# Kernel optimization log

Hardware: AMD Instinct MI355X
Metric: run time of the kernel (lower is better)

Reference implementation:

```python
import jax, jax.numpy as jnp
import numpy as np

# sign with straight-through estimator: grad passes only where |input| < 1
@jax.custom_vjp
def sign_ste(x):
    return jnp.sign(x)

def _sign_ste_fwd(x):
    return jnp.sign(x), x

def _sign_ste_bwd(x, g):
    return (jnp.where(jnp.abs(x) < 1.0, g, jnp.zeros_like(g)),)

sign_ste.defvjp(_sign_ste_fwd, _sign_ste_bwd)

# weight binarization: torch mutates weight.data in-place, so autograd treats
# sign() as identity w.r.t. the weight variable (plain linear gradient)
@jax.custom_vjp
def sign_id(w):
    return jnp.sign(w)

def _sign_id_fwd(w):
    return jnp.sign(w), None

def _sign_id_bwd(_, g):
    return (g,)

sign_id.defvjp(_sign_id_fwd, _sign_id_bwd)


def setup_inputs() -> dict:
    key = jax.random.key(0)
    k1, k2, k3 = jax.random.split(key, 3)
    x = jax.random.normal(k1, (8192, 4096), dtype=jnp.float32)
    # weight initialized to random ±1 (bernoulli(0.5)*2-1), as in __init__
    W = jnp.sign(jax.random.normal(k2, (4096, 4096), dtype=jnp.float32))
    b = jax.random.normal(k3, (4096,), dtype=jnp.float32) * 0.02
    return {"x": x, "W": W, "b": b}


def reference(x, W, b):
    # x: [N, in]; W: [out, in]; b: [out]
    x_mean = jnp.mean(jnp.abs(x))          # scalar scale, differentiable
    xb = sign_ste(x)                        # ±1 activations, STE gradient
    wb = sign_id(W)                         # ±1 weights, identity gradient
    out = jnp.einsum('ni,oi->no', xb, wb) + b  # [N, out]
    return out * x_mean
```

## Files before the change

### kernel.cpp

```cpp
#include <hip/hip_runtime.h>

typedef int intx4 __attribute__((ext_vector_type(4)));
typedef int intx8 __attribute__((ext_vector_type(8)));
typedef float floatx4 __attribute__((ext_vector_type(4)));

#define M_DIM 8192
#define N_DIM 4096
#define K_DIM 4096
#define KB2 (K_DIM / 2)

#define PACK_BLOCKS 2048
#define NF4_X ((size_t)M_DIM * K_DIM / 4)
#define NF4_TOT (NF4_X + (size_t)N_DIM * K_DIM / 4)

__device__ __forceinline__ void gld_lds16(const char* g, char* l) {
  __builtin_amdgcn_global_load_lds(
      (const __attribute__((address_space(1))) unsigned int*)g,
      (__attribute__((address_space(3))) unsigned int*)l,
      16, 0, 0);
}

__device__ __forceinline__ unsigned nib(float v) {
  return v > 0.0f ? 0x2u : (v < 0.0f ? 0xAu : 0x0u);
}

__global__ __launch_bounds__(256) void pack_kernel(const float* __restrict__ x,
                                                   const float* __restrict__ Wm,
                                                   unsigned short* __restrict__ pk,
                                                   double* __restrict__ accd) {
  const int t = threadIdx.x;
  const size_t stride = (size_t)PACK_BLOCKS * 256;
  const float4* __restrict__ X4 = (const float4*)x;
  const float4* __restrict__ W4 = (const float4*)Wm;
  float s = 0.0f;
  for (size_t i = (size_t)blockIdx.x * 256 + t; i < NF4_TOT; i += stride) {
    float4 v;
    if (i < NF4_X) {
      v = X4[i];
      s += fabsf(v.x) + fabsf(v.y) + fabsf(v.z) + fabsf(v.w);
    } else {
      v = W4[i - NF4_X];
    }
    pk[i] = (unsigned short)(nib(v.x) | (nib(v.y) << 4) | (nib(v.z) << 8) |
                             (nib(v.w) << 12));
  }
  #pragma unroll
  for (int off = 32; off > 0; off >>= 1) s += __shfl_down(s, off);
  __shared__ float sp[4];
  if ((t & 63) == 0) sp[t >> 6] = s;
  __syncthreads();
  if (t == 0) atomicAdd(accd, (double)(sp[0] + sp[1] + sp[2] + sp[3]));
}

__global__ __launch_bounds__(256) void gemm_kernel(const char* __restrict__ Xb,
                                                   const char* __restrict__ Wb,
                                                   const float* __restrict__ bias,
                                                   const double* __restrict__ accd,
                                                   float* __restrict__ out) {
  __shared__ __align__(16) char lA[2][8192];
  __shared__ __align__(16) char lB[2][8192];
  const int t = threadIdx.x;
  const int lane = t & 63;
  const int w = t >> 6;
  const int m16 = lane & 15;
  const int quad = lane >> 4;
  const int bM = blockIdx.y * 128;
  const int bN = blockIdx.x * 128;
  const int waveM = (w & 1) * 64;
  const int waveN = (w >> 1) * 64;

  const int srl = 2 * (t >> 3) + (t & 1);
  const int ssc = (t >> 1) & 3;
  const int g0 = (ssc + (srl >> 1)) & 3;
  const char* gA = Xb + (size_t)(bM + srl) * KB2 + g0 * 16;
  const char* gB = Wb + (size_t)(bN + srl) * KB2 + g0 * 16;
  const int ldst = w * 1024;

  int offA[4], offB[4];
  #pragma unroll
  for (int i = 0; i < 4; ++i) {
    const int m = waveM + i * 16 + m16;
    offA[i] = (m >> 1) * 128 + (((quad - (m >> 1)) & 3)) * 32 + (m & 1) * 16;
    const int n = waveN + i * 16 + m16;
    offB[i] = (n >> 1) * 128 + (((quad - (n >> 1)) & 3)) * 32 + (n & 1) * 16;
  }

  floatx4 acc[4][4];
  #pragma unroll
  for (int i = 0; i < 4; ++i)
    #pragma unroll
    for (int j = 0; j < 4; ++j)
      acc[i][j] = (floatx4){0.0f, 0.0f, 0.0f, 0.0f};

#define STAGE(BUF, KB)                                                      \
  do {                                                                      \
    gld_lds16(gA + (KB), &lA[BUF][ldst]);                                   \
    gld_lds16(gA + (KB) + (size_t)64 * KB2, &lA[BUF][4096 + ldst]);         \
    gld_lds16(gB + (KB), &lB[BUF][ldst]);                                   \
    gld_lds16(gB + (KB) + (size_t)64 * KB2, &lB[BUF][4096 + ldst]);         \
  } while (0)

#define COMPUTE(BUF)                                                        \
  do {                                                                      \
    intx8 a8[4];                                                            \
    _Pragma("unroll")                                                       \
    for (int i = 0; i < 4; ++i) {                                           \
      intx4 lo = *(const intx4*)&lA[BUF][offA[i]];                          \
      a8[i] = (intx8){lo[0], lo[1], lo[2], lo[3], 0, 0, 0, 0};              \
    }                                                                       \
    _Pragma("unroll")                                                       \
    for (int j = 0; j < 4; ++j) {                                           \
      intx4 lo = *(const intx4*)&lB[BUF][offB[j]];                          \
      intx8 b8 = (intx8){lo[0], lo[1], lo[2], lo[3], 0, 0, 0, 0};           \
      _Pragma("unroll")                                                     \
      for (int i = 0; i < 4; ++i)                                           \
        acc[i][j] = __builtin_amdgcn_mfma_scale_f32_16x16x128_f8f6f4(       \
            a8[i], b8, acc[i][j], 4, 4, 0, 0x7F7F7F7F, 0, 0x7F7F7F7F);      \
    }                                                                       \
  } while (0)

  STAGE(0, 0);
  __syncthreads();

  for (int kt = 0; kt < K_DIM; kt += 256) {
    const size_t kb = (size_t)(kt >> 1);
    STAGE(1, kb + 64);
    COMPUTE(0);
    __syncthreads();
    if (kt + 256 < K_DIM) STAGE(0, kb + 128);
    COMPUTE(1);
    __syncthreads();
  }
#undef STAGE
#undef COMPUTE

  const float scale = (float)(*accd * (1.0 / (double)((size_t)M_DIM * K_DIM)));

  #pragma unroll
  for (int j = 0; j < 4; ++j) {
    const int col = bN + waveN + j * 16 + m16;
    const float bj = bias[col];
    #pragma unroll
    for (int i = 0; i < 4; ++i) {
      const size_t row0 = (size_t)(bM + waveM + i * 16 + quad * 4);
      float* po = out + row0 * N_DIM + col;
      #pragma unroll
      for (int r = 0; r < 4; ++r)
        po[(size_t)r * N_DIM] = (acc[i][j][r] + bj) * scale;
    }
  }
}

extern "C" void kernel_launch(void* const* d_in, const int* in_sizes, int n_in,
                              void* d_out, int out_size, void* d_ws, size_t ws_size,
                              hipStream_t stream) {
  const float* x = (const float*)d_in[0];
  const float* W = (const float*)d_in[1];
  const float* b = (const float*)d_in[2];
  float* out = (float*)d_out;

  double* accd = (double*)d_ws;
  char* Xb = (char*)d_ws + 256;
  char* Wb = (char*)d_ws + 256 + (size_t)M_DIM * K_DIM / 2;

  hipMemsetAsync(d_ws, 0, 8, stream);
  pack_kernel<<<PACK_BLOCKS, 256, 0, stream>>>(x, W, (unsigned short*)Xb, accd);
  gemm_kernel<<<dim3(N_DIM / 128, M_DIM / 128), 256, 0, stream>>>(Xb, Wb, b, accd, out);
}
```

Before: 358.2 us.

## Enlarge GEMM tile to 256x256 with 512 threads and 4-stage LDS pipeline

The GEMM block tile grows from 128x128 to 256x256 with 8 waves, each computing a 128x64 sub-tile, which raises operand reuse per LDS load. The double-buffered loop becomes a 4-buffer async global-to-LDS pipeline using explicit vmcnt waits and raw barriers, so loads are issued three tiles ahead. MFMA sections are wrapped in s_setprio to favour matrix issue. LDS use rises to 128KB per block and the accumulator register footprint doubles, which may limit occupancy despite the launch bounds of 2.

```diff
diff --git a/kernel.cpp b/kernel.cpp
--- a/kernel.cpp
+++ b/kernel.cpp
@@ -52,22 +52,22 @@
   if (t == 0) atomicAdd(accd, (double)(sp[0] + sp[1] + sp[2] + sp[3]));
 }
 
-__global__ __launch_bounds__(256) void gemm_kernel(const char* __restrict__ Xb,
-                                                   const char* __restrict__ Wb,
-                                                   const float* __restrict__ bias,
-                                                   const double* __restrict__ accd,
-                                                   float* __restrict__ out) {
-  __shared__ __align__(16) char lA[2][8192];
-  __shared__ __align__(16) char lB[2][8192];
+__global__ __launch_bounds__(512, 2) void gemm_kernel(const char* __restrict__ Xb,
+                                                      const char* __restrict__ Wb,
+                                                      const float* __restrict__ bias,
+                                                      const double* __restrict__ accd,
+                                                      float* __restrict__ out) {
+  __shared__ __align__(16) char lA[4][16384];
+  __shared__ __align__(16) char lB[4][16384];
   const int t = threadIdx.x;
   const int lane = t & 63;
   const int w = t >> 6;
   const int m16 = lane & 15;
   const int quad = lane >> 4;
-  const int bM = blockIdx.y * 128;
-  const int bN = blockIdx.x * 128;
-  const int waveM = (w & 1) * 64;
-  const int waveN = (w >> 1) * 64;
+  const int bM = blockIdx.y * 256;
+  const int bN = blockIdx.x * 256;
+  const int waveM = (w >> 2) * 128;
+  const int waveN = (w & 3) * 64;
 
   const int srl = 2 * (t >> 3) + (t & 1);
   const int ssc = (t >> 1) & 3;
@@ -76,63 +76,78 @@
   const char* gB = Wb + (size_t)(bN + srl) * KB2 + g0 * 16;
   const int ldst = w * 1024;
 
-  int offA[4], offB[4];
+  int offA[8], offB[4];
   #pragma unroll
-  for (int i = 0; i < 4; ++i) {
+  for (int i = 0; i < 8; ++i) {
     const int m = waveM + i * 16 + m16;
     offA[i] = (m >> 1) * 128 + (((quad - (m >> 1)) & 3)) * 32 + (m & 1) * 16;
-    const int n = waveN + i * 16 + m16;
-    offB[i] = (n >> 1) * 128 + (((quad - (n >> 1)) & 3)) * 32 + (n & 1) * 16;
+  }
+  #pragma unroll
+  for (int j = 0; j < 4; ++j) {
+    const int n = waveN + j * 16 + m16;
+    offB[j] = (n >> 1) * 128 + (((quad - (n >> 1)) & 3)) * 32 + (n & 1) * 16;
   }
 
-  floatx4 acc[4][4];
+  floatx4 acc[8][4];
   #pragma unroll
-  for (int i = 0; i < 4; ++i)
+  for (int i = 0; i < 8; ++i)
     #pragma unroll
     for (int j = 0; j < 4; ++j)
       acc[i][j] = (floatx4){0.0f, 0.0f, 0.0f, 0.0f};
 
-#define STAGE(BUF, KB)                                                      \
+#define STAGE(BUF, TILE)                                                    \
   do {                                                                      \
-    gld_lds16(gA + (KB), &lA[BUF][ldst]);                                   \
-    gld_lds16(gA + (KB) + (size_t)64 * KB2, &lA[BUF][4096 + ldst]);         \
-    gld_lds16(gB + (KB), &lB[BUF][ldst]);                                   \
-    gld_lds16(gB + (KB) + (size_t)64 * KB2, &lB[BUF][4096 + ldst]);         \
+    const size_t kb = (size_t)(TILE) * 64;                                  \
+    gld_lds16(gA + kb, &lA[BUF][ldst]);                                     \
+    gld_lds16(gA + kb + (size_t)128 * KB2, &lA[BUF][8192 + ldst]);          \
+    gld_lds16(gB + kb, &lB[BUF][ldst]);                                     \
+    gld_lds16(gB + kb + (size_t)128 * KB2, &lB[BUF][8192 + ldst]);          \
   } while (0)
 
 #define COMPUTE(BUF)                                                        \
   do {                                                                      \
-    intx8 a8[4];                                                            \
-    _Pragma("unroll")                                                       \
-    for (int i = 0; i < 4; ++i) {                                           \
-      intx4 lo = *(const intx4*)&lA[BUF][offA[i]];                          \
-      a8[i] = (intx8){lo[0], lo[1], lo[2], lo[3], 0, 0, 0, 0};              \
-    }                                                                       \
+    intx8 b8[4];                                                            \
     _Pragma("unroll")                                                       \
     for (int j = 0; j < 4; ++j) {                                           \
       intx4 lo = *(const intx4*)&lB[BUF][offB[j]];                          \
-      intx8 b8 = (intx8){lo[0], lo[1], lo[2], lo[3], 0, 0, 0, 0};           \
+      b8[j] = (intx8){lo[0], lo[1], lo[2], lo[3], 0, 0, 0, 0};              \
+    }                                                                       \
+    __builtin_amdgcn_s_setprio(1);                                          \
+    _Pragma("unroll")                                                       \
+    for (int i = 0; i < 8; ++i) {                                           \
+      intx4 lo = *(const intx4*)&lA[BUF][offA[i]];                          \
+      intx8 a8 = (intx8){lo[0], lo[1], lo[2], lo[3], 0, 0, 0, 0};           \
       _Pragma("unroll")                                                     \
-      for (int i = 0; i < 4; ++i)                                           \
+      for (int j = 0; j < 4; ++j)                                           \
         acc[i][j] = __builtin_amdgcn_mfma_scale_f32_16x16x128_f8f6f4(       \
-            a8[i], b8, acc[i][j], 4, 4, 0, 0x7F7F7F7F, 0, 0x7F7F7F7F);      \
+            a8, b8[j], acc[i][j], 4, 4, 0, 0x7F7F7F7F, 0, 0x7F7F7F7F);      \
     }                                                                       \
+    __builtin_amdgcn_s_setprio(0);                                          \
   } while (0)
 
+#define WAITV(N) asm volatile("s_waitcnt vmcnt(" #N ")" ::: "memory")
+#define FENCE() asm volatile("" ::: "memory")
+#define BAR() __builtin_amdgcn_s_barrier()
+
   STAGE(0, 0);
-  __syncthreads();
+  STAGE(1, 1);
+  STAGE(2, 2);
 
-  for (int kt = 0; kt < K_DIM; kt += 256) {
-    const size_t kb = (size_t)(kt >> 1);
-    STAGE(1, kb + 64);
-    COMPUTE(0);
-    __syncthreads();
-    if (kt + 256 < K_DIM) STAGE(0, kb + 128);
-    COMPUTE(1);
-    __syncthreads();
+  for (int b = 0; b < 28; b += 4) {
+    STAGE(3, b + 3); WAITV(12); BAR(); FENCE(); COMPUTE(0); FENCE(); BAR();
+    STAGE(0, b + 4); WAITV(12); BAR(); FENCE(); COMPUTE(1); FENCE(); BAR();
+    STAGE(1, b + 5); WAITV(12); BAR(); FENCE(); COMPUTE(2); FENCE(); BAR();
+    STAGE(2, b + 6); WAITV(12); BAR(); FENCE(); COMPUTE(3); FENCE(); BAR();
   }
+  STAGE(3, 31); WAITV(12); BAR(); FENCE(); COMPUTE(0); FENCE(); BAR();
+  WAITV(8);  BAR(); FENCE(); COMPUTE(1); FENCE(); BAR();
+  WAITV(4);  BAR(); FENCE(); COMPUTE(2); FENCE(); BAR();
+  WAITV(0);  BAR(); FENCE(); COMPUTE(3);
 #undef STAGE
 #undef COMPUTE
+#undef WAITV
+#undef FENCE
+#undef BAR
 
   const float scale = (float)(*accd * (1.0 / (double)((size_t)M_DIM * K_DIM)));
 
@@ -141,7 +156,7 @@
     const int col = bN + waveN + j * 16 + m16;
     const float bj = bias[col];
     #pragma unroll
-    for (int i = 0; i < 4; ++i) {
+    for (int i = 0; i < 8; ++i) {
       const size_t row0 = (size_t)(bM + waveM + i * 16 + quad * 4);
       float* po = out + row0 * N_DIM + col;
       #pragma unroll
@@ -165,5 +180,5 @@
 
   hipMemsetAsync(d_ws, 0, 8, stream);
   pack_kernel<<<PACK_BLOCKS, 256, 0, stream>>>(x, W, (unsigned short*)Xb, accd);
-  gemm_kernel<<<dim3(N_DIM / 128, M_DIM / 128), 256, 0, stream>>>(Xb, Wb, b, accd, out);
+  gemm_kernel<<<dim3(N_DIM / 256, M_DIM / 256), 512, 0, stream>>>(Xb, Wb, b, accd, out);
 }
```

After: 352.2 us. About the same (-1.7%).
